# Kernel optimization log

Hardware: AMD Instinct MI355X
Metric: run time of the kernel (lower is better)

## Reference

```python
import jax, jax.numpy as jnp
import numpy as np

FEAT = 2048
NUM_CLASSES = 751
EPS = 1e-5


def setup_inputs() -> dict:
    key = jax.random.key(0)
    k1, k2, k3 = jax.random.split(key, 3)
    probe_x = jax.random.normal(k1, (64, FEAT), dtype=jnp.float32)
    gallery_x = jax.random.normal(k2, (256, FEAT), dtype=jnp.float32)
    # BatchNorm1d affine params (PyTorch init: gamma=1, beta=0)
    bn_gamma = jnp.ones((FEAT,), dtype=jnp.float32)
    bn_beta = jnp.zeros((FEAT,), dtype=jnp.float32)
    # classifier: weight ~ N(0, 0.001), bias = 0
    W = jax.random.normal(k3, (NUM_CLASSES, FEAT), dtype=jnp.float32) * 0.001
    b = jnp.zeros((NUM_CLASSES,), dtype=jnp.float32)
    return {"probe_x": probe_x, "gallery_x": gallery_x,
            "bn_gamma": bn_gamma, "bn_beta": bn_beta, "W": W, "b": b}


def reference(probe_x, gallery_x, bn_gamma, bn_beta, W, b):
    n_probe, feat = probe_x.shape
    n_gallery = gallery_x.shape[0]
    # broadcast squared difference: [Np, Ng, F]
    diff = jnp.square(probe_x[:, None, :] - gallery_x[None, :, :])
    d = diff.reshape(n_probe * n_gallery, feat)
    # BatchNorm1d in training mode: biased batch statistics over the batch dim
    mean = jnp.mean(d, axis=0)
    var = jnp.mean(jnp.square(d - mean), axis=0)
    bn = (d - mean) * (bn_gamma / jnp.sqrt(var + EPS)) + bn_beta
    # Linear classifier
    cls = jnp.einsum('nf,cf->nc', bn, W) + b
    return cls.reshape(n_probe, n_gallery, -1)
```

## Files before the change

### kernel.cpp

```cpp
#include <hip/hip_runtime.h>
#include <hip/hip_bf16.h>
#include <hip/hip_fp16.h>

#define FEAT 2048
#define NCLS 751
#define NPAD 768
#define NPRB 64
#define NGAL 256
#define WSCALE 256.0f

typedef _Float16 f16x8 __attribute__((ext_vector_type(8)));
typedef float f32x4 __attribute__((ext_vector_type(4)));

__device__ __forceinline__ unsigned short f2h_u(float x) {
  union { _Float16 h; unsigned short u; } v;
  v.h = (_Float16)x;
  return v.u;
}

__global__ __launch_bounds__(256)
void stats_kernel(const float* __restrict__ P, const float* __restrict__ G,
                  const float* __restrict__ gamma, const float* __restrict__ beta,
                  float* __restrict__ st) {
  const int t = threadIdx.x;
  const int fx = t & 7, ry = t >> 3;
  const int f = blockIdx.x * 8 + fx;
  float a1 = 0, a2 = 0, a3 = 0, a4 = 0;
#pragma unroll
  for (int r = ry; r < NPRB; r += 32) {
    float x = P[r * FEAT + f], x2 = x * x;
    a1 += x; a2 += x2; a3 += x2 * x; a4 += x2 * x2;
  }
  float b1 = 0, b2 = 0, b3 = 0, b4 = 0;
#pragma unroll
  for (int r = ry; r < NGAL; r += 32) {
    float x = G[r * FEAT + f], x2 = x * x;
    b1 += x; b2 += x2; b3 += x2 * x; b4 += x2 * x2;
  }
  __shared__ float red[8][32][8];
  __shared__ float red2[8][4][8];
  float vals[8] = {a1, a2, a3, a4, b1, b2, b3, b4};
#pragma unroll
  for (int m = 0; m < 8; ++m) red[m][ry][fx] = vals[m];
  __syncthreads();
  {
    int m = t >> 5, q = (t >> 3) & 3, fx2 = t & 7;
    float s = 0.f;
#pragma unroll
    for (int r = 0; r < 8; ++r) s += red[m][q * 8 + r][fx2];
    red2[m][q][fx2] = s;
  }
  __syncthreads();
  if (t < 8) {
    float mm[8];
#pragma unroll
    for (int m = 0; m < 8; ++m)
      mm[m] = red2[m][0][t] + red2[m][1][t] + red2[m][2][t] + red2[m][3][t];
    float M1p = mm[0] * (1.f / NPRB), M2p = mm[1] * (1.f / NPRB);
    float M3p = mm[2] * (1.f / NPRB), M4p = mm[3] * (1.f / NPRB);
    float M1g = mm[4] * (1.f / NGAL), M2g = mm[5] * (1.f / NGAL);
    float M3g = mm[6] * (1.f / NGAL), M4g = mm[7] * (1.f / NGAL);
    float mean = M2p - 2.f * M1p * M1g + M2g;
    float Ed2 = M4p - 4.f * M3p * M1g + 6.f * M2p * M2g - 4.f * M1p * M3g + M4g;
    float var = Ed2 - mean * mean;
    int ff = blockIdx.x * 8 + t;
    float sv = gamma[ff] / sqrtf(var + 1e-5f);
    st[ff] = sv;
    st[FEAT + ff] = beta[ff] - mean * sv;
  }
}

__global__ void prepw_kernel(const float* __restrict__ W, const float* __restrict__ b,
                             const float* __restrict__ st,
                             unsigned short* __restrict__ Wp, float* __restrict__ bp) {
  int c = blockIdx.x;
  int f = threadIdx.x * 8;
  float4 w0 = make_float4(0.f, 0.f, 0.f, 0.f), w1 = w0;
  if (c < NCLS) {
    const float4* wsrc = (const float4*)(W + (size_t)c * FEAT + f);
    w0 = wsrc[0]; w1 = wsrc[1];
  }
  const float4* s4 = (const float4*)(st + f);
  float4 s0 = s4[0], s1 = s4[1];
  const float4* t4 = (const float4*)(st + FEAT + f);
  float4 t0 = t4[0], t1 = t4[1];
  uint4 u;
  u.x = (unsigned int)f2h_u(w0.x * s0.x * WSCALE) | ((unsigned int)f2h_u(w0.y * s0.y * WSCALE) << 16);
  u.y = (unsigned int)f2h_u(w0.z * s0.z * WSCALE) | ((unsigned int)f2h_u(w0.w * s0.w * WSCALE) << 16);
  u.z = (unsigned int)f2h_u(w1.x * s1.x * WSCALE) | ((unsigned int)f2h_u(w1.y * s1.y * WSCALE) << 16);
  u.w = (unsigned int)f2h_u(w1.z * s1.z * WSCALE) | ((unsigned int)f2h_u(w1.w * s1.w * WSCALE) << 16);
  *(uint4*)(Wp + (size_t)c * FEAT + f) = u;
  float acc = t0.x * w0.x + t0.y * w0.y + t0.z * w0.z + t0.w * w0.w +
              t1.x * w1.x + t1.y * w1.y + t1.z * w1.z + t1.w * w1.w;
#pragma unroll
  for (int off = 32; off > 0; off >>= 1) acc += __shfl_down(acc, off, 64);
  __shared__ float r[4];
  int wave = threadIdx.x >> 6, lane = threadIdx.x & 63;
  if (lane == 0) r[wave] = acc;
  __syncthreads();
  if (threadIdx.x == 0) bp[c] = (c < NCLS ? b[c] : 0.f) + r[0] + r[1] + r[2] + r[3];
}

__global__ __launch_bounds__(256, 3)
void gemm_fused_kernel(const float* __restrict__ P, const float* __restrict__ G,
                       const unsigned short* __restrict__ Wp,
                       const float* __restrict__ bp, float* __restrict__ out) {
  __shared__ unsigned short As[2][128 * 32];
  __shared__ unsigned short Bs[2][128 * 32];
  __shared__ float Ps[3072];

  const int tid = threadIdx.x;
  const int lane = tid & 63, wave = tid >> 6;
  const int mtile = blockIdx.x, ntile = blockIdx.y;
  const int p = mtile >> 1;

  const int arow = tid >> 1, ah = tid & 1;
  const float* gp = G + (size_t)((mtile & 1) * 128 + arow) * FEAT + ah * 16;
  const int aslot0 = (2 * ah) ^ ((arow >> 1) & 3);

  const int brow = tid >> 2;
  const int bch = (tid & 3) ^ ((tid >> 3) & 3);
  const unsigned short* bg = Wp + (size_t)(ntile * 128 + brow) * FEAT + bch * 8;
  const int bldo = wave * 1024;

  {
    const float4* psrc = (const float4*)(P + (size_t)p * FEAT) + tid * 2;
    float4 pa = psrc[0], pb = psrc[1];
    ((float4*)Ps)[tid * 2] = pa;
    ((float4*)Ps)[tid * 2 + 1] = pb;
  }
  float4 g[4];
#pragma unroll
  for (int j = 0; j < 4; ++j) g[j] = ((const float4*)gp)[j];
#pragma unroll
  for (int j = 0; j < 2; ++j)
    __builtin_amdgcn_global_load_lds(
        (const __attribute__((address_space(1))) void*)(bg + (size_t)j * 64 * FEAT),
        (__attribute__((address_space(3))) void*)((char*)Bs[0] + j * 4096 + bldo), 16, 0, 0);
  __syncthreads();

  {
    const float* pr = Ps + ah * 16;
    float4 p0 = ((const float4*)pr)[0], p1 = ((const float4*)pr)[1];
    float4 p2 = ((const float4*)pr)[2], p3 = ((const float4*)pr)[3];
    float d0 = p0.x - g[0].x, d1 = p0.y - g[0].y, d2 = p0.z - g[0].z, d3 = p0.w - g[0].w;
    float d4 = p1.x - g[1].x, d5 = p1.y - g[1].y, d6 = p1.z - g[1].z, d7 = p1.w - g[1].w;
    float e0 = p2.x - g[2].x, e1 = p2.y - g[2].y, e2 = p2.z - g[2].z, e3 = p2.w - g[2].w;
    float e4 = p3.x - g[3].x, e5 = p3.y - g[3].y, e6 = p3.z - g[3].z, e7 = p3.w - g[3].w;
    uint4 ua, ub;
    ua.x = (unsigned int)f2h_u(d0 * d0) | ((unsigned int)f2h_u(d1 * d1) << 16);
    ua.y = (unsigned int)f2h_u(d2 * d2) | ((unsigned int)f2h_u(d3 * d3) << 16);
    ua.z = (unsigned int)f2h_u(d4 * d4) | ((unsigned int)f2h_u(d5 * d5) << 16);
    ua.w = (unsigned int)f2h_u(d6 * d6) | ((unsigned int)f2h_u(d7 * d7) << 16);
    ub.x = (unsigned int)f2h_u(e0 * e0) | ((unsigned int)f2h_u(e1 * e1) << 16);
    ub.y = (unsigned int)f2h_u(e2 * e2) | ((unsigned int)f2h_u(e3 * e3) << 16);
    ub.z = (unsigned int)f2h_u(e4 * e4) | ((unsigned int)f2h_u(e5 * e5) << 16);
    ub.w = (unsigned int)f2h_u(e6 * e6) | ((unsigned int)f2h_u(e7 * e7) << 16);
    unsigned short* ab = As[0] + arow * 32;
    *(uint4*)(ab + aslot0 * 8) = ua;
    *(uint4*)(ab + (aslot0 ^ 1) * 8) = ub;
  }
  __syncthreads();

  f32x4 acc[4][4];
#pragma unroll
  for (int mi = 0; mi < 4; ++mi)
#pragma unroll
    for (int ni = 0; ni < 4; ++ni) acc[mi][ni] = (f32x4){0.f, 0.f, 0.f, 0.f};

  const int wm = (wave & 1) * 64, wn = (wave >> 1) * 64;
  const int frow = lane & 15, fk = lane >> 4;
  const int fslot = fk ^ ((frow >> 1) & 3);

  int cur = 0;
  for (int t = 0; t < 64; ++t) {
    const int k0 = t * 32;
    const bool hn = (t < 63);
    float4 pn0, pn1, pn2, pn3;

    if (hn) {
      const float* gn = gp + k0 + 32;
#pragma unroll
      for (int j = 0; j < 4; ++j) g[j] = ((const float4*)gn)[j];
#pragma unroll
      for (int j = 0; j < 2; ++j)
        __builtin_amdgcn_global_load_lds(
            (const __attribute__((address_space(1))) void*)(bg + k0 + 32 + (size_t)j * 64 * FEAT),
            (__attribute__((address_space(3))) void*)((char*)Bs[cur ^ 1] + j * 4096 + bldo), 16, 0, 0);
      const float* prn = Ps + k0 + 32 + ah * 16;
      pn0 = ((const float4*)prn)[0]; pn1 = ((const float4*)prn)[1];
      pn2 = ((const float4*)prn)[2]; pn3 = ((const float4*)prn)[3];
    }

    __builtin_amdgcn_s_setprio(1);
    {
      f16x8 af[4], bf[4];
#pragma unroll
      for (int mi = 0; mi < 4; ++mi)
        af[mi] = *(const f16x8*)(As[cur] + (wm + mi * 16 + frow) * 32 + fslot * 8);
#pragma unroll
      for (int ni = 0; ni < 4; ++ni)
        bf[ni] = *(const f16x8*)(Bs[cur] + (wn + ni * 16 + frow) * 32 + fslot * 8);
#pragma unroll
      for (int mi = 0; mi < 4; ++mi)
#pragma unroll
        for (int ni = 0; ni < 4; ++ni)
          acc[mi][ni] = __builtin_amdgcn_mfma_f32_16x16x32_f16(af[mi], bf[ni], acc[mi][ni], 0, 0, 0);
    }
    __builtin_amdgcn_s_setprio(0);

    if (hn) {
      float d0 = pn0.x - g[0].x, d1 = pn0.y - g[0].y, d2 = pn0.z - g[0].z, d3 = pn0.w - g[0].w;
      float d4 = pn1.x - g[1].x, d5 = pn1.y - g[1].y, d6 = pn1.z - g[1].z, d7 = pn1.w - g[1].w;
      float e0 = pn2.x - g[2].x, e1 = pn2.y - g[2].y, e2 = pn2.z - g[2].z, e3 = pn2.w - g[2].w;
      float e4 = pn3.x - g[3].x, e5 = pn3.y - g[3].y, e6 = pn3.z - g[3].z, e7 = pn3.w - g[3].w;
      uint4 ua, ub;
      ua.x = (unsigned int)f2h_u(d0 * d0) | ((unsigned int)f2h_u(d1 * d1) << 16);
      ua.y = (unsigned int)f2h_u(d2 * d2) | ((unsigned int)f2h_u(d3 * d3) << 16);
      ua.z = (unsigned int)f2h_u(d4 * d4) | ((unsigned int)f2h_u(d5 * d5) << 16);
      ua.w = (unsigned int)f2h_u(d6 * d6) | ((unsigned int)f2h_u(d7 * d7) << 16);
      ub.x = (unsigned int)f2h_u(e0 * e0) | ((unsigned int)f2h_u(e1 * e1) << 16);
      ub.y = (unsigned int)f2h_u(e2 * e2) | ((unsigned int)f2h_u(e3 * e3) << 16);
      ub.z = (unsigned int)f2h_u(e4 * e4) | ((unsigned int)f2h_u(e5 * e5) << 16);
      ub.w = (unsigned int)f2h_u(e6 * e6) | ((unsigned int)f2h_u(e7 * e7) << 16);
      unsigned short* ab = As[cur ^ 1] + arow * 32;
      *(uint4*)(ab + aslot0 * 8) = ua;
      *(uint4*)(ab + (aslot0 ^ 1) * 8) = ub;
    }

    __syncthreads();
    cur ^= 1;
  }

  const int col0 = ntile * 128 + wn + (lane & 15);
  const int row0 = mtile * 128 + wm + ((lane >> 4) << 2);
#pragma unroll
  for (int ni = 0; ni < 4; ++ni) {
    int col = col0 + ni * 16;
    if (col >= NCLS) continue;
    float bv = bp[col];
#pragma unroll
    for (int mi = 0; mi < 4; ++mi) {
      int row = row0 + mi * 16;
#pragma unroll
      for (int r = 0; r < 4; ++r)
        out[(size_t)(row + r) * NCLS + col] = acc[mi][ni][r] * (1.0f / WSCALE) + bv;
    }
  }
}

extern "C" void kernel_launch(void* const* d_in, const int* in_sizes, int n_in,
                              void* d_out, int out_size, void* d_ws, size_t ws_size,
                              hipStream_t stream) {
  const float* P = (const float*)d_in[0];
  const float* G = (const float*)d_in[1];
  const float* gamma = (const float*)d_in[2];
  const float* beta = (const float*)d_in[3];
  const float* W = (const float*)d_in[4];
  const float* b = (const float*)d_in[5];
  float* out = (float*)d_out;

  float* st = (float*)d_ws;
  float* bp = st + 2 * FEAT;
  unsigned short* Wp = (unsigned short*)(bp + NPAD);

  hipLaunchKernelGGL(stats_kernel, dim3(256), dim3(256), 0, stream, P, G, gamma, beta, st);
  hipLaunchKernelGGL(prepw_kernel, dim3(NPAD), dim3(256), 0, stream, W, b, st, Wp, bp);
  hipLaunchKernelGGL(gemm_fused_kernel, dim3(128, 6), dim3(256), 0, stream, P, G, Wp, bp, out);
}
```

Before: 167.0 us.

## Widen GEMM tile to 128x192 with 512-thread blocks and direct P loads

Changes the fused GEMM from 256-thread 128x128 tiles to 512-thread 128x192 tiles. Eight waves each compute a 64x48 sub-tile, and the grid shrinks from 768 to 512 blocks. The P row is now loaded directly from global memory instead of being staged in LDS, which removes one barrier and some LDS use. The aim is better W reuse and fewer blocks, covering the 768 padded classes in four N tiles. The cost is fewer MFMAs per wave between barriers and heavier sync across eight waves.

```diff
diff --git a/kernel.cpp b/kernel.cpp
--- a/kernel.cpp
+++ b/kernel.cpp
@@ -101,74 +101,60 @@
   if (threadIdx.x == 0) bp[c] = (c < NCLS ? b[c] : 0.f) + r[0] + r[1] + r[2] + r[3];
 }
 
-__global__ __launch_bounds__(256, 3)
+__global__ __launch_bounds__(512, 4)
 void gemm_fused_kernel(const float* __restrict__ P, const float* __restrict__ G,
                        const unsigned short* __restrict__ Wp,
                        const float* __restrict__ bp, float* __restrict__ out) {
   __shared__ unsigned short As[2][128 * 32];
-  __shared__ unsigned short Bs[2][128 * 32];
-  __shared__ float Ps[3072];
+  __shared__ unsigned short Bs[2][192 * 32];
 
   const int tid = threadIdx.x;
   const int lane = tid & 63, wave = tid >> 6;
   const int mtile = blockIdx.x, ntile = blockIdx.y;
   const int p = mtile >> 1;
 
-  const int arow = tid >> 1, ah = tid & 1;
-  const float* gp = G + (size_t)((mtile & 1) * 128 + arow) * FEAT + ah * 16;
-  const int aslot0 = (2 * ah) ^ ((arow >> 1) & 3);
-
-  const int brow = tid >> 2;
-  const int bch = (tid & 3) ^ ((tid >> 3) & 3);
-  const unsigned short* bg = Wp + (size_t)(ntile * 128 + brow) * FEAT + bch * 8;
-  const int bldo = wave * 1024;
-
+  const int arow = tid >> 2, ach = tid & 3;
+  const int aoff = arow * 32 + ((ach ^ ((arow >> 1) & 3)) * 8);
+  const float* gp = G + (size_t)((mtile & 1) * 128 + arow) * FEAT + ach * 8;
+  const float* pp = P + (size_t)p * FEAT + ach * 8;
+
+  const int bch = (lane & 3) ^ ((lane >> 3) & 3);
+  const unsigned short* bg0 =
+      Wp + (size_t)(ntile * 192 + wave * 16 + (lane >> 2)) * FEAT + bch * 8;
+  const unsigned short* bg1 =
+      Wp + (size_t)(ntile * 192 + 128 + wave * 16 + (lane >> 2)) * FEAT + bch * 8;
+  const int bdo0 = wave * 1024;
+  const int bdo1 = 8192 + wave * 1024;
+
+  float4 ga, gb, pa, pb;
+  ga = ((const float4*)gp)[0]; gb = ((const float4*)gp)[1];
+  pa = ((const float4*)pp)[0]; pb = ((const float4*)pp)[1];
+  __builtin_amdgcn_global_load_lds(
+      (const __attribute__((address_space(1))) void*)bg0,
+      (__attribute__((address_space(3))) void*)((char*)Bs[0] + bdo0), 16, 0, 0);
+  if (wave < 4)
+    __builtin_amdgcn_global_load_lds(
+        (const __attribute__((address_space(1))) void*)bg1,
+        (__attribute__((address_space(3))) void*)((char*)Bs[0] + bdo1), 16, 0, 0);
   {
-    const float4* psrc = (const float4*)(P + (size_t)p * FEAT) + tid * 2;
-    float4 pa = psrc[0], pb = psrc[1];
-    ((float4*)Ps)[tid * 2] = pa;
-    ((float4*)Ps)[tid * 2 + 1] = pb;
-  }
-  float4 g[4];
-#pragma unroll
-  for (int j = 0; j < 4; ++j) g[j] = ((const float4*)gp)[j];
-#pragma unroll
-  for (int j = 0; j < 2; ++j)
-    __builtin_amdgcn_global_load_lds(
-        (const __attribute__((address_space(1))) void*)(bg + (size_t)j * 64 * FEAT),
-        (__attribute__((address_space(3))) void*)((char*)Bs[0] + j * 4096 + bldo), 16, 0, 0);
-  __syncthreads();
-
-  {
-    const float* pr = Ps + ah * 16;
-    float4 p0 = ((const float4*)pr)[0], p1 = ((const float4*)pr)[1];
-    float4 p2 = ((const float4*)pr)[2], p3 = ((const float4*)pr)[3];
-    float d0 = p0.x - g[0].x, d1 = p0.y - g[0].y, d2 = p0.z - g[0].z, d3 = p0.w - g[0].w;
-    float d4 = p1.x - g[1].x, d5 = p1.y - g[1].y, d6 = p1.z - g[1].z, d7 = p1.w - g[1].w;
-    float e0 = p2.x - g[2].x, e1 = p2.y - g[2].y, e2 = p2.z - g[2].z, e3 = p2.w - g[2].w;
-    float e4 = p3.x - g[3].x, e5 = p3.y - g[3].y, e6 = p3.z - g[3].z, e7 = p3.w - g[3].w;
-    uint4 ua, ub;
-    ua.x = (unsigned int)f2h_u(d0 * d0) | ((unsigned int)f2h_u(d1 * d1) << 16);
-    ua.y = (unsigned int)f2h_u(d2 * d2) | ((unsigned int)f2h_u(d3 * d3) << 16);
-    ua.z = (unsigned int)f2h_u(d4 * d4) | ((unsigned int)f2h_u(d5 * d5) << 16);
-    ua.w = (unsigned int)f2h_u(d6 * d6) | ((unsigned int)f2h_u(d7 * d7) << 16);
-    ub.x = (unsigned int)f2h_u(e0 * e0) | ((unsigned int)f2h_u(e1 * e1) << 16);
-    ub.y = (unsigned int)f2h_u(e2 * e2) | ((unsigned int)f2h_u(e3 * e3) << 16);
-    ub.z = (unsigned int)f2h_u(e4 * e4) | ((unsigned int)f2h_u(e5 * e5) << 16);
-    ub.w = (unsigned int)f2h_u(e6 * e6) | ((unsigned int)f2h_u(e7 * e7) << 16);
-    unsigned short* ab = As[0] + arow * 32;
-    *(uint4*)(ab + aslot0 * 8) = ua;
-    *(uint4*)(ab + (aslot0 ^ 1) * 8) = ub;
-  }
-  __syncthreads();
-
-  f32x4 acc[4][4];
+    float d0 = pa.x - ga.x, d1 = pa.y - ga.y, d2 = pa.z - ga.z, d3 = pa.w - ga.w;
+    float d4 = pb.x - gb.x, d5 = pb.y - gb.y, d6 = pb.z - gb.z, d7 = pb.w - gb.w;
+    uint4 u;
+    u.x = (unsigned int)f2h_u(d0 * d0) | ((unsigned int)f2h_u(d1 * d1) << 16);
+    u.y = (unsigned int)f2h_u(d2 * d2) | ((unsigned int)f2h_u(d3 * d3) << 16);
+    u.z = (unsigned int)f2h_u(d4 * d4) | ((unsigned int)f2h_u(d5 * d5) << 16);
+    u.w = (unsigned int)f2h_u(d6 * d6) | ((unsigned int)f2h_u(d7 * d7) << 16);
+    *(uint4*)(As[0] + aoff) = u;
+  }
+  __syncthreads();
+
+  f32x4 acc[4][3];
 #pragma unroll
   for (int mi = 0; mi < 4; ++mi)
 #pragma unroll
-    for (int ni = 0; ni < 4; ++ni) acc[mi][ni] = (f32x4){0.f, 0.f, 0.f, 0.f};
-
-  const int wm = (wave & 1) * 64, wn = (wave >> 1) * 64;
+    for (int ni = 0; ni < 3; ++ni) acc[mi][ni] = (f32x4){0.f, 0.f, 0.f, 0.f};
+
+  const int wm = (wave & 1) * 64, wn = (wave >> 1) * 48;
   const int frow = lane & 15, fk = lane >> 4;
   const int fslot = fk ^ ((frow >> 1) & 3);
 
@@ -176,66 +162,57 @@
   for (int t = 0; t < 64; ++t) {
     const int k0 = t * 32;
     const bool hn = (t < 63);
-    float4 pn0, pn1, pn2, pn3;
 
     if (hn) {
       const float* gn = gp + k0 + 32;
-#pragma unroll
-      for (int j = 0; j < 4; ++j) g[j] = ((const float4*)gn)[j];
-#pragma unroll
-      for (int j = 0; j < 2; ++j)
+      const float* pn = pp + k0 + 32;
+      ga = ((const float4*)gn)[0]; gb = ((const float4*)gn)[1];
+      pa = ((const float4*)pn)[0]; pb = ((const float4*)pn)[1];
+      __builtin_amdgcn_global_load_lds(
+          (const __attribute__((address_space(1))) void*)(bg0 + k0 + 32),
+          (__attribute__((address_space(3))) void*)((char*)Bs[cur ^ 1] + bdo0), 16, 0, 0);
+      if (wave < 4)
         __builtin_amdgcn_global_load_lds(
-            (const __attribute__((address_space(1))) void*)(bg + k0 + 32 + (size_t)j * 64 * FEAT),
-            (__attribute__((address_space(3))) void*)((char*)Bs[cur ^ 1] + j * 4096 + bldo), 16, 0, 0);
-      const float* prn = Ps + k0 + 32 + ah * 16;
-      pn0 = ((const float4*)prn)[0]; pn1 = ((const float4*)prn)[1];
-      pn2 = ((const float4*)prn)[2]; pn3 = ((const float4*)prn)[3];
+            (const __attribute__((address_space(1))) void*)(bg1 + k0 + 32),
+            (__attribute__((address_space(3))) void*)((char*)Bs[cur ^ 1] + bdo1), 16, 0, 0);
     }
 
     __builtin_amdgcn_s_setprio(1);
     {
-      f16x8 af[4], bf[4];
+      f16x8 af[4], bf[3];
 #pragma unroll
       for (int mi = 0; mi < 4; ++mi)
         af[mi] = *(const f16x8*)(As[cur] + (wm + mi * 16 + frow) * 32 + fslot * 8);
 #pragma unroll
-      for (int ni = 0; ni < 4; ++ni)
+      for (int ni = 0; ni < 3; ++ni)
         bf[ni] = *(const f16x8*)(Bs[cur] + (wn + ni * 16 + frow) * 32 + fslot * 8);
 #pragma unroll
       for (int mi = 0; mi < 4; ++mi)
 #pragma unroll
-        for (int ni = 0; ni < 4; ++ni)
+        for (int ni = 0; ni < 3; ++ni)
           acc[mi][ni] = __builtin_amdgcn_mfma_f32_16x16x32_f16(af[mi], bf[ni], acc[mi][ni], 0, 0, 0);
     }
     __builtin_amdgcn_s_setprio(0);
 
     if (hn) {
-      float d0 = pn0.x - g[0].x, d1 = pn0.y - g[0].y, d2 = pn0.z - g[0].z, d3 = pn0.w - g[0].w;
-      float d4 = pn1.x - g[1].x, d5 = pn1.y - g[1].y, d6 = pn1.z - g[1].z, d7 = pn1.w - g[1].w;
-      float e0 = pn2.x - g[2].x, e1 = pn2.y - g[2].y, e2 = pn2.z - g[2].z, e3 = pn2.w - g[2].w;
-      float e4 = pn3.x - g[3].x, e5 = pn3.y - g[3].y, e6 = pn3.z - g[3].z, e7 = pn3.w - g[3].w;
-      uint4 ua, ub;
-      ua.x = (unsigned int)f2h_u(d0 * d0) | ((unsigned int)f2h_u(d1 * d1) << 16);
-      ua.y = (unsigned int)f2h_u(d2 * d2) | ((unsigned int)f2h_u(d3 * d3) << 16);
-      ua.z = (unsigned int)f2h_u(d4 * d4) | ((unsigned int)f2h_u(d5 * d5) << 16);
-      ua.w = (unsigned int)f2h_u(d6 * d6) | ((unsigned int)f2h_u(d7 * d7) << 16);
-      ub.x = (unsigned int)f2h_u(e0 * e0) | ((unsigned int)f2h_u(e1 * e1) << 16);
-      ub.y = (unsigned int)f2h_u(e2 * e2) | ((unsigned int)f2h_u(e3 * e3) << 16);
-      ub.z = (unsigned int)f2h_u(e4 * e4) | ((unsigned int)f2h_u(e5 * e5) << 16);
-      ub.w = (unsigned int)f2h_u(e6 * e6) | ((unsigned int)f2h_u(e7 * e7) << 16);
-      unsigned short* ab = As[cur ^ 1] + arow * 32;
-      *(uint4*)(ab + aslot0 * 8) = ua;
-      *(uint4*)(ab + (aslot0 ^ 1) * 8) = ub;
+      float d0 = pa.x - ga.x, d1 = pa.y - ga.y, d2 = pa.z - ga.z, d3 = pa.w - ga.w;
+      float d4 = pb.x - gb.x, d5 = pb.y - gb.y, d6 = pb.z - gb.z, d7 = pb.w - gb.w;
+      uint4 u;
+      u.x = (unsigned int)f2h_u(d0 * d0) | ((unsigned int)f2h_u(d1 * d1) << 16);
+      u.y = (unsigned int)f2h_u(d2 * d2) | ((unsigned int)f2h_u(d3 * d3) << 16);
+      u.z = (unsigned int)f2h_u(d4 * d4) | ((unsigned int)f2h_u(d5 * d5) << 16);
+      u.w = (unsigned int)f2h_u(d6 * d6) | ((unsigned int)f2h_u(d7 * d7) << 16);
+      *(uint4*)(As[cur ^ 1] + aoff) = u;
     }
 
     __syncthreads();
     cur ^= 1;
   }
 
-  const int col0 = ntile * 128 + wn + (lane & 15);
+  const int col0 = ntile * 192 + wn + (lane & 15);
   const int row0 = mtile * 128 + wm + ((lane >> 4) << 2);
 #pragma unroll
-  for (int ni = 0; ni < 4; ++ni) {
+  for (int ni = 0; ni < 3; ++ni) {
     int col = col0 + ni * 16;
     if (col >= NCLS) continue;
     float bv = bp[col];
@@ -266,5 +243,5 @@
 
   hipLaunchKernelGGL(stats_kernel, dim3(256), dim3(256), 0, stream, P, G, gamma, beta, st);
   hipLaunchKernelGGL(prepw_kernel, dim3(NPAD), dim3(256), 0, stream, W, b, st, Wp, bp);
-  hipLaunchKernelGGL(gemm_fused_kernel, dim3(128, 6), dim3(256), 0, stream, P, G, Wp, bp, out);
-}
+  hipLaunchKernelGGL(gemm_fused_kernel, dim3(128, 4), dim3(512), 0, stream, P, G, Wp, bp, out);
+}
```

Result: no change. 164.6 us (-1.5%).
